# Optimization experiments

Hardware: AMD Instinct MI355X
Metric: run time of the kernel (lower is better)

The kernel has to match this reference:

```python
import jax, jax.numpy as jnp
import numpy as np

N_VARS = 1_000_000
N_CONSTRS = 1_000_000
NNZ = 16_000_000


def setup_inputs() -> dict:
    key = jax.random.key(0)
    ks = jax.random.split(key, 8)
    pred = jax.random.uniform(ks[0], (N_VARS,), dtype=jnp.float32)
    coeff = jax.random.normal(ks[1], (NNZ,), dtype=jnp.float32)
    constr_rhs = jax.random.normal(ks[2], (N_CONSTRS,), dtype=jnp.float32)
    var_lb = jax.random.normal(ks[3], (N_VARS,), dtype=jnp.float32)
    var_ub = jax.random.uniform(ks[4], (N_VARS,), dtype=jnp.float32)
    constr_idx = jnp.sort(jax.random.randint(ks[5], (NNZ,), 0, N_CONSTRS, dtype=jnp.int32))
    var_idx = jax.random.randint(ks[6], (NNZ,), 0, N_VARS, dtype=jnp.int32)
    constr_sense = jax.random.randint(ks[7], (N_CONSTRS,), 0, 4, dtype=jnp.int32)
    return {
        "pred": pred,
        "coeff": coeff,
        "constr_rhs": constr_rhs,
        "var_lb": var_lb,
        "var_ub": var_ub,
        "constr_idx": constr_idx,
        "var_idx": var_idx,
        "constr_sense": constr_sense,
        "n_vars": N_VARS,
        "n_constrs": N_CONSTRS,
    }


def reference(pred, coeff, constr_rhs, var_lb, var_ub, constr_idx, var_idx,
              constr_sense, n_vars, n_constrs):
    # Denormalize predictions from [0,1] to original variable bounds.
    values = pred * (var_ub - var_lb) + var_lb  # (n_vars,)
    # Sparse COO Ax: segmented scatter-add of coeff * x[var_idx] into rows.
    ax = jax.ops.segment_sum(coeff * values[var_idx], constr_idx,
                             num_segments=n_constrs)  # (n_constrs,)
    diff = ax - constr_rhs
    zero = jnp.zeros((), dtype=diff.dtype)
    violations = jnp.where(
        constr_sense == 1, jnp.maximum(diff, 0.0),      # <= : relu(ax - b)
        jnp.where(constr_sense == 2, jnp.maximum(-diff, 0.0),  # >= : relu(b - ax)
                  jnp.where(constr_sense == 3, jnp.abs(diff), zero)))  # == : |ax-b|
    return violations.mean()  # reduction='mean'
```

## Files before the change

### kernel.cpp

```cpp
#include <hip/hip_runtime.h>
#include <hip/hip_bf16.h>

__global__ void denorm_kernel(const float* __restrict__ pred,
                              const float* __restrict__ lb,
                              const float* __restrict__ ub,
                              float* __restrict__ values, int n) {
    int i = blockIdx.x * blockDim.x + threadIdx.x;
    if (i < n) {
        values[i] = pred[i] * (ub[i] - lb[i]) + lb[i];
    }
}

__global__ void scatter_kernel(const float* __restrict__ coeff,
                               const int* __restrict__ constr_idx,
                               const int* __restrict__ var_idx,
                               const float* __restrict__ values,
                               float* __restrict__ ax, int nnz) {
    int i = blockIdx.x * blockDim.x + threadIdx.x;
    int lane = threadIdx.x & 63;

    int seg = -1;
    float v = 0.0f;
    if (i < nnz) {
        seg = constr_idx[i];
        v = coeff[i] * values[var_idx[i]];
    }

    #pragma unroll
    for (int off = 1; off < 64; off <<= 1) {
        float ov = __shfl_up(v, off, 64);
        int   os = __shfl_up(seg, off, 64);
        if (lane >= off && os == seg) v += ov;
    }

    int nseg = __shfl_down(seg, 1, 64);
    bool is_tail = (lane == 63) || (nseg != seg);
    if (is_tail && seg >= 0) {
        atomicAdd(&ax[seg], v);
    }
}

__global__ void violation_kernel(const float* __restrict__ ax,
                                 const float* __restrict__ rhs,
                                 const int* __restrict__ sense,
                                 float* __restrict__ out,
                                 int n, float inv_n) {
    __shared__ float warp_sums[4];
    int i = blockIdx.x * blockDim.x + threadIdx.x;

    float viol = 0.0f;
    if (i < n) {
        float diff = ax[i] - rhs[i];
        int s = sense[i];
        if (s == 1)      viol = fmaxf(diff, 0.0f);
        else if (s == 2) viol = fmaxf(-diff, 0.0f);
        else if (s == 3) viol = fabsf(diff);
    }

    #pragma unroll
    for (int off = 32; off > 0; off >>= 1) {
        viol += __shfl_down(viol, off, 64);
    }
    int lane = threadIdx.x & 63;
    int wave = threadIdx.x >> 6;
    if (lane == 0) warp_sums[wave] = viol;
    __syncthreads();

    if (threadIdx.x == 0) {
        float s = warp_sums[0] + warp_sums[1] + warp_sums[2] + warp_sums[3];
        atomicAdd(out, s * inv_n);
    }
}

extern "C" void kernel_launch(void* const* d_in, const int* in_sizes, int n_in,
                              void* d_out, int out_size, void* d_ws, size_t ws_size,
                              hipStream_t stream) {
    const float* pred       = (const float*)d_in[0];
    const float* coeff      = (const float*)d_in[1];
    const float* rhs        = (const float*)d_in[2];
    const float* lb         = (const float*)d_in[3];
    const float* ub         = (const float*)d_in[4];
    const int*   constr_idx = (const int*)d_in[5];
    const int*   var_idx    = (const int*)d_in[6];
    const int*   sense      = (const int*)d_in[7];

    const int n_vars    = in_sizes[0];
    const int nnz       = in_sizes[1];
    const int n_constrs = in_sizes[2];

    float* values = (float*)d_ws;
    float* ax     = values + n_vars;
    float* out    = (float*)d_out;

    hipMemsetAsync(ax, 0, (size_t)n_constrs * sizeof(float), stream);
    hipMemsetAsync(out, 0, sizeof(float), stream);

    const int BLK = 256;
    denorm_kernel<<<(n_vars + BLK - 1) / BLK, BLK, 0, stream>>>(
        pred, lb, ub, values, n_vars);
    scatter_kernel<<<(nnz + BLK - 1) / BLK, BLK, 0, stream>>>(
        coeff, constr_idx, var_idx, values, ax, nnz);
    violation_kernel<<<(n_constrs + BLK - 1) / BLK, BLK, 0, stream>>>(
        ax, rhs, sense, out, n_constrs, 1.0f / (float)n_constrs);
}
```

Measured before the change: 358.8 us.

## Vectorize loads, fuse zeroing into denorm, per-thread segmented scatter over 16 nonzeros

Merges the two memsets into the denormalization kernel and vectorizes it and the violation kernel with float4/int4 loads. The scatter changes from a wave-wide shuffle scan with one element per thread to 16 consecutive nonzeros per thread. Each thread loads its nonzeros as nontemporal vector loads and accumulates runs of equal rows serially before issuing atomics. This cuts shuffle work and launch overhead and widens memory transactions, at the cost of more atomics per segment, since a row of about 16 entries now spans around two threads. The vectorized paths assume the vector counts are divisible by 4 and drop any tail.

```diff
diff --git a/kernel.cpp b/kernel.cpp
--- a/kernel.cpp
+++ b/kernel.cpp
@@ -1,60 +1,116 @@
 #include <hip/hip_runtime.h>
 #include <hip/hip_bf16.h>
 
-__global__ void denorm_kernel(const float* __restrict__ pred,
-                              const float* __restrict__ lb,
-                              const float* __restrict__ ub,
-                              float* __restrict__ values, int n) {
+typedef float vfloat4 __attribute__((ext_vector_type(4)));
+typedef int   vint4   __attribute__((ext_vector_type(4)));
+
+__global__ void denorm_zero_kernel(const vfloat4* __restrict__ pred,
+                                   const vfloat4* __restrict__ lb,
+                                   const vfloat4* __restrict__ ub,
+                                   vfloat4* __restrict__ values,
+                                   vfloat4* __restrict__ ax,
+                                   float* __restrict__ out,
+                                   int n4v, int n4c) {
     int i = blockIdx.x * blockDim.x + threadIdx.x;
-    if (i < n) {
-        values[i] = pred[i] * (ub[i] - lb[i]) + lb[i];
+    if (i < n4v) {
+        vfloat4 p = pred[i], l = lb[i], u = ub[i];
+        vfloat4 v;
+        v.x = fmaf(p.x, u.x - l.x, l.x);
+        v.y = fmaf(p.y, u.y - l.y, l.y);
+        v.z = fmaf(p.z, u.z - l.z, l.z);
+        v.w = fmaf(p.w, u.w - l.w, l.w);
+        values[i] = v;
+    }
+    if (i < n4c) {
+        vfloat4 z = {0.f, 0.f, 0.f, 0.f};
+        ax[i] = z;
+    }
+    if (i == 0) *out = 0.0f;
+}
+
+__global__ void scatter_kernel(const vfloat4* __restrict__ coeff,
+                               const vint4* __restrict__ cidx,
+                               const vint4* __restrict__ vidx,
+                               const float* __restrict__ values,
+                               float* __restrict__ ax,
+                               int nnz) {
+    const int K = 16;
+    int t = blockIdx.x * blockDim.x + threadIdx.x;
+    long base = (long)t * K;
+    if (base >= nnz) return;
+
+    if (base + K <= nnz) {
+        long b4 = (long)t * 4;
+        int cseg[16]; int vix[16]; float cf[16];
+        #pragma unroll
+        for (int j = 0; j < 4; j++) {
+            vint4 c = __builtin_nontemporal_load(&cidx[b4 + j]);
+            cseg[4*j+0] = c.x; cseg[4*j+1] = c.y; cseg[4*j+2] = c.z; cseg[4*j+3] = c.w;
+        }
+        #pragma unroll
+        for (int j = 0; j < 4; j++) {
+            vint4 v = __builtin_nontemporal_load(&vidx[b4 + j]);
+            vix[4*j+0] = v.x; vix[4*j+1] = v.y; vix[4*j+2] = v.z; vix[4*j+3] = v.w;
+        }
+        float vals[16];
+        #pragma unroll
+        for (int k = 0; k < 16; k++) vals[k] = values[vix[k]];
+        #pragma unroll
+        for (int j = 0; j < 4; j++) {
+            vfloat4 f = __builtin_nontemporal_load(&coeff[b4 + j]);
+            cf[4*j+0] = f.x; cf[4*j+1] = f.y; cf[4*j+2] = f.z; cf[4*j+3] = f.w;
+        }
+
+        int cur = cseg[0];
+        float acc = cf[0] * vals[0];
+        #pragma unroll
+        for (int k = 1; k < 16; k++) {
+            if (cseg[k] == cur) {
+                acc = fmaf(cf[k], vals[k], acc);
+            } else {
+                atomicAdd(&ax[cur], acc);
+                cur = cseg[k];
+                acc = cf[k] * vals[k];
+            }
+        }
+        atomicAdd(&ax[cur], acc);
+    } else {
+        const int* ci = (const int*)cidx;
+        const int* vi = (const int*)vidx;
+        const float* cf = (const float*)coeff;
+        int cur = ci[base];
+        float acc = cf[base] * values[vi[base]];
+        for (long k = base + 1; k < nnz; k++) {
+            int s = ci[k];
+            float p = cf[k] * values[vi[k]];
+            if (s == cur) acc += p;
+            else { atomicAdd(&ax[cur], acc); cur = s; acc = p; }
+        }
+        atomicAdd(&ax[cur], acc);
     }
 }
 
-__global__ void scatter_kernel(const float* __restrict__ coeff,
-                               const int* __restrict__ constr_idx,
-                               const int* __restrict__ var_idx,
-                               const float* __restrict__ values,
-                               float* __restrict__ ax, int nnz) {
-    int i = blockIdx.x * blockDim.x + threadIdx.x;
-    int lane = threadIdx.x & 63;
-
-    int seg = -1;
-    float v = 0.0f;
-    if (i < nnz) {
-        seg = constr_idx[i];
-        v = coeff[i] * values[var_idx[i]];
-    }
-
-    #pragma unroll
-    for (int off = 1; off < 64; off <<= 1) {
-        float ov = __shfl_up(v, off, 64);
-        int   os = __shfl_up(seg, off, 64);
-        if (lane >= off && os == seg) v += ov;
-    }
-
-    int nseg = __shfl_down(seg, 1, 64);
-    bool is_tail = (lane == 63) || (nseg != seg);
-    if (is_tail && seg >= 0) {
-        atomicAdd(&ax[seg], v);
-    }
-}
-
-__global__ void violation_kernel(const float* __restrict__ ax,
-                                 const float* __restrict__ rhs,
-                                 const int* __restrict__ sense,
+__global__ void violation_kernel(const vfloat4* __restrict__ ax,
+                                 const vfloat4* __restrict__ rhs,
+                                 const vint4* __restrict__ sense,
                                  float* __restrict__ out,
-                                 int n, float inv_n) {
+                                 int n4, float inv_n) {
     __shared__ float warp_sums[4];
     int i = blockIdx.x * blockDim.x + threadIdx.x;
 
     float viol = 0.0f;
-    if (i < n) {
-        float diff = ax[i] - rhs[i];
-        int s = sense[i];
-        if (s == 1)      viol = fmaxf(diff, 0.0f);
-        else if (s == 2) viol = fmaxf(-diff, 0.0f);
-        else if (s == 3) viol = fabsf(diff);
+    if (i < n4) {
+        vfloat4 a = ax[i], r = rhs[i];
+        vint4 s = sense[i];
+        float d, pos, neg;
+        d = a.x - r.x; pos = fmaxf(d, 0.f); neg = fmaxf(-d, 0.f);
+        viol += (s.x == 1) ? pos : (s.x == 2) ? neg : (s.x == 3) ? (pos + neg) : 0.f;
+        d = a.y - r.y; pos = fmaxf(d, 0.f); neg = fmaxf(-d, 0.f);
+        viol += (s.y == 1) ? pos : (s.y == 2) ? neg : (s.y == 3) ? (pos + neg) : 0.f;
+        d = a.z - r.z; pos = fmaxf(d, 0.f); neg = fmaxf(-d, 0.f);
+        viol += (s.z == 1) ? pos : (s.z == 2) ? neg : (s.z == 3) ? (pos + neg) : 0.f;
+        d = a.w - r.w; pos = fmaxf(d, 0.f); neg = fmaxf(-d, 0.f);
+        viol += (s.w == 1) ? pos : (s.w == 2) ? neg : (s.w == 3) ? (pos + neg) : 0.f;
     }
 
     #pragma unroll
@@ -92,14 +148,20 @@
     float* ax     = values + n_vars;
     float* out    = (float*)d_out;
 
-    hipMemsetAsync(ax, 0, (size_t)n_constrs * sizeof(float), stream);
-    hipMemsetAsync(out, 0, sizeof(float), stream);
+    const int BLK = 256;
 
-    const int BLK = 256;
-    denorm_kernel<<<(n_vars + BLK - 1) / BLK, BLK, 0, stream>>>(
-        pred, lb, ub, values, n_vars);
-    scatter_kernel<<<(nnz + BLK - 1) / BLK, BLK, 0, stream>>>(
-        coeff, constr_idx, var_idx, values, ax, nnz);
-    violation_kernel<<<(n_constrs + BLK - 1) / BLK, BLK, 0, stream>>>(
-        ax, rhs, sense, out, n_constrs, 1.0f / (float)n_constrs);
+    int n4v = n_vars / 4, n4c = n_constrs / 4;
+    int n4max = (n4v > n4c) ? n4v : n4c;
+    denorm_zero_kernel<<<(n4max + BLK - 1) / BLK, BLK, 0, stream>>>(
+        (const vfloat4*)pred, (const vfloat4*)lb, (const vfloat4*)ub,
+        (vfloat4*)values, (vfloat4*)ax, out, n4v, n4c);
+
+    int nchunk = (nnz + 15) / 16;
+    scatter_kernel<<<(nchunk + BLK - 1) / BLK, BLK, 0, stream>>>(
+        (const vfloat4*)coeff, (const vint4*)constr_idx, (const vint4*)var_idx,
+        values, ax, nnz);
+
+    violation_kernel<<<(n4c + BLK - 1) / BLK, BLK, 0, stream>>>(
+        (const vfloat4*)ax, (const vfloat4*)rhs, (const vint4*)sense,
+        out, n4c, 1.0f / (float)n_constrs);
 }
```

Result: faster. 320.0 us (-10.8%).
